# Kernel tuning notes

Measured on AMD Instinct MI355X. Metric: run time of the kernel, lower is better.

## Reference

```python
import jax, jax.numpy as jnp
import numpy as np

B, L, NIN, NHID, NLAYERS = 16, 2048, 1024, 1024, 2


def _gru_step_zero_h(x, W_ih, b_ih, W_hh, b_hh):
    """torch GRU cell with h_prev = 0 (faithful to the module's bug where
    hidden is never updated and starts at zeros).
    r = sigmoid(W_ir x + b_ir + b_hr)
    z = sigmoid(W_iz x + b_iz + b_hz)
    n = tanh(W_in x + b_in + r * b_hn)   # W_hn @ 0 == 0
    h = (1 - z) * n                       # + z * 0
    W_hh is unused because h_prev == 0 (kept as an arg for parity).
    """
    del W_hh
    g = jnp.einsum('blf,hf->blh', x, W_ih) + b_ih  # (B, L, 3H)
    H = b_ih.shape[0] // 3
    gi_r, gi_z, gi_n = g[..., :H], g[..., H:2 * H], g[..., 2 * H:]
    bh_r, bh_z, bh_n = b_hh[:H], b_hh[H:2 * H], b_hh[2 * H:]
    r = jax.nn.sigmoid(gi_r + bh_r)
    z = jax.nn.sigmoid(gi_z + bh_z)
    n = jnp.tanh(gi_n + r * bh_n)
    return (1.0 - z) * n


def setup_inputs() -> dict:
    key = jax.random.key(0)
    ks = jax.random.split(key, 12)
    s_in = 1.0 / np.sqrt(NIN)
    s_h = 1.0 / np.sqrt(NHID)
    inp = {
        'inputs': jax.random.normal(ks[0], (B, L, NIN), dtype=jnp.float32),
        'inputs_mask': jax.random.randint(ks[1], (B, L), 0, 2, dtype=jnp.int32),
        # layer 0 (input size NIN)
        'W_ih0': jax.random.uniform(ks[2], (3 * NHID, NIN), jnp.float32, -s_in, s_in),
        'W_hh0': jax.random.uniform(ks[3], (3 * NHID, NHID), jnp.float32, -s_h, s_h),
        'b_ih0': jax.random.uniform(ks[4], (3 * NHID,), jnp.float32, -s_h, s_h),
        'b_hh0': jax.random.uniform(ks[5], (3 * NHID,), jnp.float32, -s_h, s_h),
        # layer 1 (input size NHID)
        'W_ih1': jax.random.uniform(ks[6], (3 * NHID, NHID), jnp.float32, -s_h, s_h),
        'W_hh1': jax.random.uniform(ks[7], (3 * NHID, NHID), jnp.float32, -s_h, s_h),
        'b_ih1': jax.random.uniform(ks[8], (3 * NHID,), jnp.float32, -s_h, s_h),
        'b_hh1': jax.random.uniform(ks[9], (3 * NHID,), jnp.float32, -s_h, s_h),
    }
    return inp


def reference(inputs, inputs_mask, W_ih0, W_hh0, b_ih0, b_hh0,
              W_ih1, W_hh1, b_ih1, b_hh1):
    # hidden is never updated in the original step(), so every timestep runs
    # the 2-layer GRU one step from zero hidden -> fully parallel over time.
    h1 = _gru_step_zero_h(inputs, W_ih0, b_ih0, W_hh0, b_hh0)   # (B, L, H)
    h2 = _gru_step_zero_h(h1, W_ih1, b_ih1, W_hh1, b_hh1)       # (B, L, H)
    mask = inputs_mask.astype(h2.dtype)[..., None]               # (B, L, 1)
    # output_p * mask + hidden[0] * (1 - mask), with hidden[0] == 0
    out = h2 * mask
    # original returns (steps, b_s, nhid)
    return jnp.transpose(out, (1, 0, 2))
```

## Files before the change

### kernel.cpp

```cpp
#include <hip/hip_runtime.h>
#include <hip/hip_bf16.h>
#include <cstdint>
#include <cstddef>

#define BB 16
#define LL 2048
#define MM (BB * LL)
#define KK 1024
#define HH 1024

typedef __attribute__((ext_vector_type(8))) short bf16x8;
typedef __attribute__((ext_vector_type(4))) float f32x4;

__device__ __forceinline__ unsigned short f2bf(float f) {
    unsigned u = __builtin_bit_cast(unsigned, f);
    u += 0x7fffu + ((u >> 16) & 1u);
    return (unsigned short)(u >> 16);
}

__global__ void cvt_f32_to_bf16(const float* __restrict__ in,
                                unsigned short* __restrict__ out, int n8) {
    int i = blockIdx.x * blockDim.x + threadIdx.x;
    if (i >= n8) return;
    const float4* p = reinterpret_cast<const float4*>(in) + (size_t)i * 2;
    float4 v0 = p[0];
    float4 v1 = p[1];
    union { unsigned short us[8]; uint4 v; } o;
    o.us[0] = f2bf(v0.x); o.us[1] = f2bf(v0.y);
    o.us[2] = f2bf(v0.z); o.us[3] = f2bf(v0.w);
    o.us[4] = f2bf(v1.x); o.us[5] = f2bf(v1.y);
    o.us[6] = f2bf(v1.z); o.us[7] = f2bf(v1.w);
    reinterpret_cast<uint4*>(out)[i] = o.v;
}

__global__ __launch_bounds__(1024) void scan_mask(const int* __restrict__ mask,
                                                  int* __restrict__ rows,
                                                  int* __restrict__ Na) {
    __shared__ int psum[1024];
    const int t = threadIdx.x;
    const int base = t * 32;
    int m[32];
    int cnt = 0;
#pragma unroll
    for (int i = 0; i < 32; ++i) { m[i] = mask[base + i]; cnt += (m[i] != 0); }
    psum[t] = cnt;
    __syncthreads();
    for (int off = 1; off < 1024; off <<= 1) {
        int v = (t >= off) ? psum[t - off] : 0;
        __syncthreads();
        psum[t] += v;
        __syncthreads();
    }
    int offset = psum[t] - cnt;
#pragma unroll
    for (int i = 0; i < 32; ++i) {
        if (m[i]) rows[offset++] = base + i;
    }
    if (t == 1023) *Na = psum[1023];
}

__global__ __launch_bounds__(256) void gather_cvt(const float* __restrict__ x,
                                                  const int* __restrict__ rows,
                                                  const int* __restrict__ Na,
                                                  unsigned short* __restrict__ xbf) {
    const int j = blockIdx.x;
    if (j >= *Na) return;
    const int r = rows[j];
    const float4 v = reinterpret_cast<const float4*>(x + (size_t)r * KK)[threadIdx.x];
    ushort4 o;
    o.x = f2bf(v.x); o.y = f2bf(v.y); o.z = f2bf(v.z); o.w = f2bf(v.w);
    reinterpret_cast<ushort4*>(xbf + (size_t)j * KK)[threadIdx.x] = o;
}

__global__ __launch_bounds__(256) void zero_masked(const int* __restrict__ mask,
                                                   float* __restrict__ out) {
    const int m = blockIdx.x;
    if (mask[m] != 0) return;
    const int bb = m >> 11;
    const int ll = m & 2047;
    float4 z = {0.f, 0.f, 0.f, 0.f};
    reinterpret_cast<float4*>(out + ((size_t)ll * BB + bb) * HH)[threadIdx.x] = z;
}

__device__ __forceinline__ void gload16(const unsigned short* g, unsigned short* l) {
    __builtin_amdgcn_global_load_lds(
        (const __attribute__((address_space(1))) unsigned int*)g,
        (__attribute__((address_space(3))) unsigned int*)l,
        16, 0, 0);
}

#define WAITVM0  asm volatile("s_waitcnt vmcnt(0)" ::: "memory")
#define SB       __builtin_amdgcn_sched_barrier(0)
#define BAR      __builtin_amdgcn_s_barrier()

template <int MODE>
__global__ __launch_bounds__(256, 3) void gru_layer(
    const unsigned short* __restrict__ A,
    const unsigned short* __restrict__ W,
    const float* __restrict__ b_ih,
    const float* __restrict__ b_hh,
    const int* __restrict__ rows,
    const int* __restrict__ Na_p,
    unsigned short* __restrict__ out_bf,
    float* __restrict__ out_f) {
    __shared__ unsigned short lds[2][10240];

    const int Na = *Na_p;
    const int m0 = blockIdx.x * 128;
    if (m0 >= Na) return;
    const int n0 = blockIdx.y * 64;

    const int tid  = threadIdx.x;
    const int lane = tid & 63;
    const int wid  = tid >> 6;
    const int wr   = wid >> 1;
    const int wc   = wid & 1;

    const int trow = tid >> 2;
    const int tcol = ((tid & 3) ^ ((trow >> 1) & 3)) * 8;
    int r0 = m0 + trow;        if (r0 >= Na) r0 = Na - 1;
    int r1 = m0 + 64 + trow;   if (r1 >= Na) r1 = Na - 1;
    const unsigned short* a0 = A + (size_t)r0 * KK + tcol;
    const unsigned short* a1 = A + (size_t)r1 * KK + tcol;
    const unsigned short* b0 = W + (size_t)(0 * HH + n0 + trow) * KK + tcol;
    const unsigned short* b1 = W + (size_t)(1 * HH + n0 + trow) * KK + tcol;
    const unsigned short* b2 = W + (size_t)(2 * HH + n0 + trow) * KK + tcol;

#define STAGE(kt, c) do {                                        \
        const int _o = (kt) * 32;                                \
        unsigned short* _L = &lds[(c)][wid * 512];               \
        gload16(a0 + _o, _L + 0 * 2048);                         \
        gload16(a1 + _o, _L + 1 * 2048);                         \
        gload16(b0 + _o, _L + 2 * 2048);                         \
        gload16(b1 + _o, _L + 3 * 2048);                         \
        gload16(b2 + _o, _L + 4 * 2048);                         \
    } while (0)

    const int l15 = lane & 15;
    const int akp = (((lane >> 4) ^ (lane >> 1)) & 3) << 3;
    int aoff[4], boff[2];
#pragma unroll
    for (int mf = 0; mf < 4; ++mf)
        aoff[mf] = (wr * 64 + mf * 16 + l15) * 32 + akp;
#pragma unroll
    for (int nf = 0; nf < 2; ++nf)
        boff[nf] = 4096 + (wc * 32 + nf * 16 + l15) * 32 + akp;

    f32x4 accr[4][2] = {};
    f32x4 accz[4][2] = {};
    f32x4 accn[4][2] = {};

#define COMPUTE(Lp) do {                                                          \
        bf16x8 af[4];                                                             \
        _Pragma("unroll") for (int mf = 0; mf < 4; ++mf)                          \
            af[mf] = *reinterpret_cast<const bf16x8*>(&(Lp)[aoff[mf]]);           \
        _Pragma("unroll") for (int nf = 0; nf < 2; ++nf) {                        \
            bf16x8 br  = *reinterpret_cast<const bf16x8*>(&(Lp)[boff[nf]]);       \
            bf16x8 bz  = *reinterpret_cast<const bf16x8*>(&(Lp)[boff[nf] + 2048]);\
            bf16x8 bnn = *reinterpret_cast<const bf16x8*>(&(Lp)[boff[nf] + 4096]);\
            __builtin_amdgcn_s_setprio(1);                                        \
            _Pragma("unroll") for (int mf = 0; mf < 4; ++mf) {                    \
                accr[mf][nf] = __builtin_amdgcn_mfma_f32_16x16x32_bf16(           \
                    af[mf], br,  accr[mf][nf], 0, 0, 0);                          \
                accz[mf][nf] = __builtin_amdgcn_mfma_f32_16x16x32_bf16(           \
                    af[mf], bz,  accz[mf][nf], 0, 0, 0);                          \
                accn[mf][nf] = __builtin_amdgcn_mfma_f32_16x16x32_bf16(           \
                    af[mf], bnn, accn[mf][nf], 0, 0, 0);                          \
            }                                                                     \
            __builtin_amdgcn_s_setprio(0);                                        \
        }                                                                         \
    } while (0)

    STAGE(0, 0);
    WAITVM0; BAR; SB;

    int cur = 0;
#pragma unroll 1
    for (int kt = 0; kt < 31; ++kt) {
        STAGE(kt + 1, cur ^ 1);
        const unsigned short* L = &lds[cur][0];
        COMPUTE(L);
        WAITVM0; BAR; SB;
        cur ^= 1;
    }
    {
        const unsigned short* L = &lds[cur][0];
        COMPUTE(L);
    }

#pragma unroll
    for (int nf = 0; nf < 2; ++nf) {
        const int col = n0 + wc * 32 + nf * 16 + l15;
        const float br_b = b_ih[col] + b_hh[col];
        const float bz_b = b_ih[HH + col] + b_hh[HH + col];
        const float bn_i = b_ih[2 * HH + col];
        const float bn_h = b_hh[2 * HH + col];
#pragma unroll
        for (int mf = 0; mf < 4; ++mf) {
#pragma unroll
            for (int j = 0; j < 4; ++j) {
                const int row = m0 + wr * 64 + mf * 16 + (lane >> 4) * 4 + j;
                if (row >= Na) continue;
                const float r = 1.f / (1.f + __expf(-(accr[mf][nf][j] + br_b)));
                const float z = 1.f / (1.f + __expf(-(accz[mf][nf][j] + bz_b)));
                const float n = tanhf(accn[mf][nf][j] + bn_i + r * bn_h);
                const float h = (1.f - z) * n;
                if (MODE == 0) {
                    out_bf[(size_t)row * HH + col] = f2bf(h);
                } else {
                    const int orig = rows[row];
                    const int bb = orig >> 11;
                    const int ll = orig & 2047;
                    out_f[((size_t)ll * BB + bb) * HH + col] = h;
                }
            }
        }
    }
#undef STAGE
#undef COMPUTE
}

extern "C" void kernel_launch(void* const* d_in, const int* in_sizes, int n_in,
                              void* d_out, int out_size, void* d_ws, size_t ws_size,
                              hipStream_t stream) {
    const float* x   = (const float*)d_in[0];
    const int*   msk = (const int*)d_in[1];
    const float* W0  = (const float*)d_in[2];
    const float* bi0 = (const float*)d_in[4];
    const float* bh0 = (const float*)d_in[5];
    const float* W1  = (const float*)d_in[6];
    const float* bi1 = (const float*)d_in[8];
    const float* bh1 = (const float*)d_in[9];
    float* out = (float*)d_out;

    char* ws = (char*)d_ws;
    unsigned short* xbf  = (unsigned short*)ws;
    unsigned short* h1bf = (unsigned short*)(ws + 67108864);
    unsigned short* w0bf = (unsigned short*)(ws + 134217728);
    unsigned short* w1bf = (unsigned short*)(ws + 140509184);
    int* rows = (int*)(ws + 146800640);
    int* Na   = (int*)(ws + 146931712);

    scan_mask<<<1, 1024, 0, stream>>>(msk, rows, Na);

    cvt_f32_to_bf16<<<1536, 256, 0, stream>>>(W0, w0bf, 3 * HH * KK / 8);
    cvt_f32_to_bf16<<<1536, 256, 0, stream>>>(W1, w1bf, 3 * HH * KK / 8);

    zero_masked<<<MM, 256, 0, stream>>>(msk, out);
    gather_cvt<<<MM, 256, 0, stream>>>(x, rows, Na, xbf);

    dim3 grid(MM / 128, HH / 64);
    gru_layer<0><<<grid, 256, 0, stream>>>(xbf, w0bf, bi0, bh0, rows, Na, h1bf, nullptr);
    gru_layer<1><<<grid, 256, 0, stream>>>(h1bf, w1bf, bi1, bh1, rows, Na, nullptr, out);
}
```

Baseline: 348.6 us.

## Load GEMM A operand straight to registers, stage only weights in LDS

The activation (A) tile is no longer staged through LDS. Each wave loads its own A fragments from global memory straight into double-buffered registers, and only the three gate weight tiles go through LDS, which shrinks the shared-memory footprint. The wait changes to vmcnt(4) so the register A loads can stay in flight while the LDS loads complete. The occupancy hint drops from 3 to 2 and tanhf is replaced with an exp-based formula. The two column-waves now fetch the same A rows twice, and the A global loads are less coalesced.

```diff
diff --git a/kernel.cpp b/kernel.cpp
--- a/kernel.cpp
+++ b/kernel.cpp
@@ -89,12 +89,12 @@
         16, 0, 0);
 }
 
-#define WAITVM0  asm volatile("s_waitcnt vmcnt(0)" ::: "memory")
+#define WAITVM4  asm volatile("s_waitcnt vmcnt(4)" ::: "memory")
 #define SB       __builtin_amdgcn_sched_barrier(0)
 #define BAR      __builtin_amdgcn_s_barrier()
 
 template <int MODE>
-__global__ __launch_bounds__(256, 3) void gru_layer(
+__global__ __launch_bounds__(256, 2) void gru_layer(
     const unsigned short* __restrict__ A,
     const unsigned short* __restrict__ W,
     const float* __restrict__ b_ih,
@@ -103,7 +103,7 @@
     const int* __restrict__ Na_p,
     unsigned short* __restrict__ out_bf,
     float* __restrict__ out_f) {
-    __shared__ unsigned short lds[2][10240];
+    __shared__ unsigned short lds[2][6144];
 
     const int Na = *Na_p;
     const int m0 = blockIdx.x * 128;
@@ -118,10 +118,6 @@
 
     const int trow = tid >> 2;
     const int tcol = ((tid & 3) ^ ((trow >> 1) & 3)) * 8;
-    int r0 = m0 + trow;        if (r0 >= Na) r0 = Na - 1;
-    int r1 = m0 + 64 + trow;   if (r1 >= Na) r1 = Na - 1;
-    const unsigned short* a0 = A + (size_t)r0 * KK + tcol;
-    const unsigned short* a1 = A + (size_t)r1 * KK + tcol;
     const unsigned short* b0 = W + (size_t)(0 * HH + n0 + trow) * KK + tcol;
     const unsigned short* b1 = W + (size_t)(1 * HH + n0 + trow) * KK + tcol;
     const unsigned short* b2 = W + (size_t)(2 * HH + n0 + trow) * KK + tcol;
@@ -129,31 +125,36 @@
 #define STAGE(kt, c) do {                                        \
         const int _o = (kt) * 32;                                \
         unsigned short* _L = &lds[(c)][wid * 512];               \
-        gload16(a0 + _o, _L + 0 * 2048);                         \
-        gload16(a1 + _o, _L + 1 * 2048);                         \
-        gload16(b0 + _o, _L + 2 * 2048);                         \
-        gload16(b1 + _o, _L + 3 * 2048);                         \
-        gload16(b2 + _o, _L + 4 * 2048);                         \
+        gload16(b0 + _o, _L + 0 * 2048);                         \
+        gload16(b1 + _o, _L + 1 * 2048);                         \
+        gload16(b2 + _o, _L + 2 * 2048);                         \
     } while (0)
 
     const int l15 = lane & 15;
+    const unsigned short* aptr[4];
+#pragma unroll
+    for (int mf = 0; mf < 4; ++mf) {
+        int r = m0 + wr * 64 + mf * 16 + l15;
+        if (r >= Na) r = Na - 1;
+        aptr[mf] = A + (size_t)r * KK + (lane >> 4) * 8;
+    }
+#define LOADA(dst, kt) do {                                                    \
+        _Pragma("unroll") for (int mf = 0; mf < 4; ++mf)                       \
+            dst[mf] = *reinterpret_cast<const bf16x8*>(aptr[mf] + (kt) * 32);  \
+    } while (0)
+
     const int akp = (((lane >> 4) ^ (lane >> 1)) & 3) << 3;
-    int aoff[4], boff[2];
-#pragma unroll
-    for (int mf = 0; mf < 4; ++mf)
-        aoff[mf] = (wr * 64 + mf * 16 + l15) * 32 + akp;
+    int boff[2];
 #pragma unroll
     for (int nf = 0; nf < 2; ++nf)
-        boff[nf] = 4096 + (wc * 32 + nf * 16 + l15) * 32 + akp;
+        boff[nf] = (wc * 32 + nf * 16 + l15) * 32 + akp;
 
     f32x4 accr[4][2] = {};
     f32x4 accz[4][2] = {};
     f32x4 accn[4][2] = {};
-
-#define COMPUTE(Lp) do {                                                          \
-        bf16x8 af[4];                                                             \
-        _Pragma("unroll") for (int mf = 0; mf < 4; ++mf)                          \
-            af[mf] = *reinterpret_cast<const bf16x8*>(&(Lp)[aoff[mf]]);           \
+    bf16x8 afA[4], afB[4];
+
+#define COMPUTE(Lp, af) do {                                                      \
         _Pragma("unroll") for (int nf = 0; nf < 2; ++nf) {                        \
             bf16x8 br  = *reinterpret_cast<const bf16x8*>(&(Lp)[boff[nf]]);       \
             bf16x8 bz  = *reinterpret_cast<const bf16x8*>(&(Lp)[boff[nf] + 2048]);\
@@ -172,21 +173,25 @@
     } while (0)
 
     STAGE(0, 0);
-    WAITVM0; BAR; SB;
-
-    int cur = 0;
+    LOADA(afA, 0);
+    WAITVM4; BAR; SB;
+
 #pragma unroll 1
-    for (int kt = 0; kt < 31; ++kt) {
-        STAGE(kt + 1, cur ^ 1);
-        const unsigned short* L = &lds[cur][0];
-        COMPUTE(L);
-        WAITVM0; BAR; SB;
-        cur ^= 1;
-    }
-    {
-        const unsigned short* L = &lds[cur][0];
-        COMPUTE(L);
-    }
+    for (int kt = 0; kt < 30; kt += 2) {
+        STAGE(kt + 1, 1);
+        LOADA(afB, kt + 1);
+        COMPUTE(lds[0], afA);
+        WAITVM4; BAR; SB;
+        STAGE(kt + 2, 0);
+        LOADA(afA, kt + 2);
+        COMPUTE(lds[1], afB);
+        WAITVM4; BAR; SB;
+    }
+    STAGE(31, 1);
+    LOADA(afB, 31);
+    COMPUTE(lds[0], afA);
+    WAITVM4; BAR; SB;
+    COMPUTE(lds[1], afB);
 
 #pragma unroll
     for (int nf = 0; nf < 2; ++nf) {
@@ -203,8 +208,10 @@
                 if (row >= Na) continue;
                 const float r = 1.f / (1.f + __expf(-(accr[mf][nf][j] + br_b)));
                 const float z = 1.f / (1.f + __expf(-(accz[mf][nf][j] + bz_b)));
-                const float n = tanhf(accn[mf][nf][j] + bn_i + r * bn_h);
-                const float h = (1.f - z) * n;
+                const float xn = accn[mf][nf][j] + bn_i + r * bn_h;
+                const float t  = __expf(-2.f * fabsf(xn));
+                const float nv = copysignf((1.f - t) / (1.f + t), xn);
+                const float h = (1.f - z) * nv;
                 if (MODE == 0) {
                     out_bf[(size_t)row * HH + col] = f2bf(h);
                 } else {
@@ -217,6 +224,7 @@
         }
     }
 #undef STAGE
+#undef LOADA
 #undef COMPUTE
 }
 
```

After: 505.0 us. +44.8%, slower.
